# Kernel tuning notes

Measured on AMD Instinct MI355X. Metric: run time of the kernel, lower is better.

## Reference

```python
import jax, jax.numpy as jnp
import numpy as np
import math

DIM = 3
N_LEVELS = 16
F = 2
LOG2 = 19
TABLE = 1 << LOG2  # 524288 entries per level
BASE, FINEST = 16, 512
_B = math.exp((math.log(FINEST) - math.log(BASE)) / (N_LEVELS - 1))
RESOLUTIONS = [math.floor(BASE * _B ** i) for i in range(N_LEVELS)]
PRIMES = np.array([1, 2654435761, 805459861], dtype=np.uint32)
K = 1 << DIM  # 8 corners
# binary_mask[k, d]: bit d of corner k is 0 -> take lower corner along dim d
MASK = (np.arange(K)[:, None] & (1 << np.arange(DIM))[None, :]) == 0

N_POINTS = 1 << 20


def setup_inputs() -> dict:
    key = jax.random.key(0)
    kx, kt = jax.random.split(key)
    x = jax.random.uniform(kx, (N_POINTS, DIM), dtype=jnp.float32)
    # nn.init.uniform_(level.weight, a=-1e-4, b=1e-4), stacked over levels
    tables = (jax.random.uniform(kt, (N_LEVELS, TABLE, F), dtype=jnp.float32) - 0.5) * 2e-4
    return {"x": x, "tables": tables}


def _level(x, table, resolution):
    """One hash-grid level: corner hash + gather + trilinear interpolation."""
    xr = x * resolution                      # [N, DIM]
    ci = xr.astype(jnp.int32)                # trunc == floor for x >= 0
    cf = xr - ci.astype(xr.dtype)            # fractional part (diff w.r.t. x)
    mask = jnp.asarray(MASK)[None]           # [1, K, DIM]
    idx = jnp.where(mask, ci[:, None, :], ci[:, None, :] + 1)          # [N, K, DIM]
    w = jnp.where(mask, 1.0 - cf[:, None, :], cf[:, None, :]).prod(-1) # [N, K]
    # fast_hash: prime multiply (mod 2^32 via uint32 wrap), XOR fold, mod table size
    hashmap_size = min(resolution ** DIM, TABLE)
    h = idx.astype(jnp.uint32) * jnp.asarray(PRIMES)                    # [N, K, DIM]
    hashed = h[..., 0]
    for d in range(1, DIM):
        hashed = hashed ^ h[..., d]
    hashed = (hashed % jnp.uint32(hashmap_size)).astype(jnp.int32)      # [N, K]
    feats = table[hashed]                                               # [N, K, F]
    return (feats * w[..., None]).sum(axis=1)                           # [N, F]


def reference(x, tables):
    outs = [_level(x, tables[l], RESOLUTIONS[l]) for l in range(N_LEVELS)]
    return jnp.concatenate(outs, axis=-1)  # [N, N_LEVELS * F]
```

## Files before the change

kernel.cpp:

```cpp
#include <hip/hip_runtime.h>
#include <cmath>
#include <cstdint>

#define NLEVELS 16
#define TABLE_SZ (1u << 19)
#define NXCD 8

typedef float f4v __attribute__((ext_vector_type(4)));
typedef uint32_t u32x4 __attribute__((ext_vector_type(4)));

struct Params {
    uint32_t res[NLEVELS];
    uint32_t size[NLEVELS];
    uint64_t magic[NLEVELS];
    int lv0[NXCD];
    int lv1[NXCD];
};

__device__ __forceinline__ float bf_lo(uint32_t v) { return __uint_as_float(v << 16); }
__device__ __forceinline__ float bf_hi(uint32_t v) { return __uint_as_float(v & 0xFFFF0000u); }

__device__ __forceinline__ uint32_t pick4(u32x4 f, uint32_t j) {
    uint32_t e01 = (j & 1) ? f[1] : f[0];
    uint32_t e23 = (j & 1) ? f[3] : f[2];
    return (j & 2) ? e23 : e01;
}

__global__ __launch_bounds__(256) void convert_kernel(
    const float* __restrict__ tab, uint32_t* __restrict__ btab, Params p)
{
    int slot = blockIdx.x & (NXCD - 1);
    uint32_t cb = blockIdx.x >> 3;
    int l0 = p.lv0[slot], l1 = p.lv1[slot];
    uint32_t n0 = p.size[l0], n1 = p.size[l1];
    uint32_t total = n0 + n1;
    uint32_t stride = (gridDim.x >> 3) * 256;
    for (uint32_t i = cb * 256 + threadIdx.x; i < total; i += stride) {
        int l; uint32_t e;
        if (i < n0) { l = l0; e = i; } else { l = l1; e = i - n0; }
        unsigned long long u = __builtin_nontemporal_load(
            (const unsigned long long*)(tab + ((size_t)l * TABLE_SZ + e) * 2));
        uint32_t bx = (uint32_t)u, by = (uint32_t)(u >> 32);
        bx = (bx + 0x7fffu + ((bx >> 16) & 1u)) >> 16;
        by = (by + 0x7fffu + ((by >> 16) & 1u)) >> 16;
        btab[(size_t)l * TABLE_SZ + e] = bx | (by << 16);
    }
}

__global__ __launch_bounds__(256) void gather_kernel(
    const float* __restrict__ x, const uint32_t* __restrict__ btab,
    float2* __restrict__ ws, int p_lo, int passN, Params p)
{
    int slot = blockIdx.x & (NXCD - 1);
    int chunk = blockIdx.x >> 3;
    int rel = chunk * 256 + threadIdx.x;
    int pt = p_lo + rel;

    float x0 = __builtin_nontemporal_load(&x[(size_t)pt * 3 + 0]);
    float x1 = __builtin_nontemporal_load(&x[(size_t)pt * 3 + 1]);
    float x2 = __builtin_nontemporal_load(&x[(size_t)pt * 3 + 2]);

#pragma unroll
    for (int t = 0; t < 2; ++t) {
        int l = t ? p.lv1[slot] : p.lv0[slot];
        uint32_t size  = p.size[l];
        uint64_t magic = p.magic[l];
        float fres = (float)p.res[l];

        float xr0 = x0 * fres, xr1 = x1 * fres, xr2 = x2 * fres;
        int ci0 = (int)xr0, ci1 = (int)xr1, ci2 = (int)xr2;
        float cf0 = xr0 - (float)ci0;
        float cf1 = xr1 - (float)ci1;
        float cf2 = xr2 - (float)ci2;

        uint32_t c0u = (uint32_t)ci0, c0v = c0u + 1u;
        uint32_t h1a = (uint32_t)ci1 * 2654435761u; uint32_t h1b = h1a + 2654435761u;
        uint32_t h2a = (uint32_t)ci2 * 805459861u;  uint32_t h2b = h2a + 805459861u;
        float w0a = 1.0f - cf0, w1a = 1.0f - cf1, w2a = 1.0f - cf2;

        const uint32_t* __restrict__ tl = btab + (size_t)l * TABLE_SZ;
        float s0 = 0.0f, s1 = 0.0f;
#pragma unroll
        for (int pq = 0; pq < 4; ++pq) {
            uint32_t tyz = ((pq & 1) ? h1b : h1a) ^ ((pq & 2) ? h2b : h2a);
            float wyz = ((pq & 1) ? cf1 : w1a) * ((pq & 2) ? cf2 : w2a);
            uint32_t hU = tyz ^ c0u;
            uint32_t hV = tyz ^ c0v;
            uint32_t rU = hU - (uint32_t)__umul64hi((uint64_t)hU, magic) * size;
            uint32_t rV = hV - (uint32_t)__umul64hi((uint64_t)hV, magic) * size;
            uint32_t base = rU & ~3u;
            u32x4 f = *reinterpret_cast<const u32x4*>(tl + base);
            uint32_t eU = pick4(f, rU & 3u);
            uint32_t eV;
            if ((rV & ~3u) == base) {
                eV = pick4(f, rV & 3u);
            } else {
                eV = tl[rV];
            }
            float wU = w0a * wyz, wV = cf0 * wyz;
            s0 = fmaf(bf_lo(eU), wU, s0);
            s1 = fmaf(bf_hi(eU), wU, s1);
            s0 = fmaf(bf_lo(eV), wV, s0);
            s1 = fmaf(bf_hi(eV), wV, s1);
        }
        unsigned long long o = (unsigned long long)__float_as_uint(s0)
                             | ((unsigned long long)__float_as_uint(s1) << 32);
        __builtin_nontemporal_store(o,
            (unsigned long long*)(ws + (size_t)l * passN + rel));
    }
}

__global__ __launch_bounds__(256) void transpose_kernel(
    const float2* __restrict__ ws, f4v* __restrict__ out4, int p_lo, int passN)
{
    __shared__ float2 lds[256 * 17];
    int base = blockIdx.x * 256;
    int tid = threadIdx.x;
#pragma unroll
    for (int l = 0; l < NLEVELS; ++l) {
        unsigned long long u = __builtin_nontemporal_load(
            (const unsigned long long*)(ws + (size_t)l * passN + base + tid));
        float2 v;
        v.x = __uint_as_float((uint32_t)u);
        v.y = __uint_as_float((uint32_t)(u >> 32));
        lds[tid * 17 + l] = v;
    }
    __syncthreads();
    size_t ob = ((size_t)(p_lo + base)) * 8;
#pragma unroll
    for (int k = 0; k < 8; ++k) {
        int flat = k * 256 + tid;
        int ptl = flat >> 3, quad = flat & 7;
        float2 a = lds[ptl * 17 + quad * 2];
        float2 b = lds[ptl * 17 + quad * 2 + 1];
        f4v o = { a.x, a.y, b.x, b.y };
        __builtin_nontemporal_store(o, out4 + ob + flat);
    }
}

__global__ __launch_bounds__(256) void hashgrid_fallback(
    const float* __restrict__ x, const float* __restrict__ tables,
    float* __restrict__ out, int n_points, Params lp)
{
    int gid = blockIdx.x * blockDim.x + threadIdx.x;
    int n = gid >> 4;
    int l = gid & 15;
    if (n >= n_points) return;
    float x0 = x[(size_t)n * 3 + 0];
    float x1 = x[(size_t)n * 3 + 1];
    float x2 = x[(size_t)n * 3 + 2];
    uint32_t size = lp.size[l];
    uint64_t magic = lp.magic[l];
    float fres = (float)lp.res[l];
    float xr0 = x0 * fres, xr1 = x1 * fres, xr2 = x2 * fres;
    int ci0 = (int)xr0, ci1 = (int)xr1, ci2 = (int)xr2;
    float cf0 = xr0 - (float)ci0, cf1 = xr1 - (float)ci1, cf2 = xr2 - (float)ci2;
    uint32_t h0a = (uint32_t)ci0;               uint32_t h0b = h0a + 1u;
    uint32_t h1a = (uint32_t)ci1 * 2654435761u; uint32_t h1b = h1a + 2654435761u;
    uint32_t h2a = (uint32_t)ci2 * 805459861u;  uint32_t h2b = h2a + 805459861u;
    float w0a = 1.0f - cf0, w1a = 1.0f - cf1, w2a = 1.0f - cf2;
    const float2* t = reinterpret_cast<const float2*>(tables) + (size_t)l * TABLE_SZ;
    float s0 = 0.0f, s1 = 0.0f;
#pragma unroll
    for (int k = 0; k < 8; ++k) {
        uint32_t h = ((k & 1) ? h0b : h0a) ^ ((k & 2) ? h1b : h1a) ^ ((k & 4) ? h2b : h2a);
        uint32_t q = (uint32_t)__umul64hi((uint64_t)h, magic);
        h -= q * size;
        float w = ((k & 1) ? cf0 : w0a) * ((k & 2) ? cf1 : w1a) * ((k & 4) ? cf2 : w2a);
        float2 f = t[h];
        s0 = fmaf(f.x, w, s0);
        s1 = fmaf(f.y, w, s1);
    }
    reinterpret_cast<float2*>(out)[(size_t)n * NLEVELS + l] = make_float2(s0, s1);
}

extern "C" void kernel_launch(void* const* d_in, const int* in_sizes, int n_in,
                              void* d_out, int out_size, void* d_ws, size_t ws_size,
                              hipStream_t stream) {
    const float* x      = (const float*)d_in[0];
    const float* tables = (const float*)d_in[1];
    float* out          = (float*)d_out;
    int n_points = in_sizes[0] / 3;

    Params p;
    double b = exp((log(512.0) - log(16.0)) / 15.0);
    for (int i = 0; i < NLEVELS; ++i) {
        double r = floor(16.0 * pow(b, (double)i));
        uint32_t res = (uint32_t)r;
        uint64_t cube = (uint64_t)res * res * res;
        uint32_t size = (cube < (uint64_t)TABLE_SZ) ? (uint32_t)cube : TABLE_SZ;
        p.res[i] = res;
        p.size[i] = size;
        p.magic[i] = ~0ULL / size + 1ULL;
    }
    for (int s = 0; s < NXCD - 1; ++s) { p.lv0[s] = 7 + s; p.lv1[s] = s; }
    p.lv0[7] = 14; p.lv1[7] = 15;

    const size_t TAB_BYTES = (size_t)NLEVELS * TABLE_SZ * 4;
    size_t rem = (ws_size > TAB_BYTES) ? ws_size - TAB_BYTES : 0;
    int passN = (int)((rem / (NLEVELS * sizeof(float2))) & ~(size_t)255);
    if (passN > n_points) passN = n_points;

    if (passN < 256 || (n_points & 255) != 0) {
        int total = n_points * NLEVELS;
        hashgrid_fallback<<<(total + 255) / 256, 256, 0, stream>>>(x, tables, out, n_points, p);
        return;
    }

    uint32_t* btab = (uint32_t*)d_ws;
    float2* wsbuf = (float2*)((char*)d_ws + TAB_BYTES);

    convert_kernel<<<128 * NXCD, 256, 0, stream>>>(tables, btab, p);

    for (int p_lo = 0; p_lo < n_points; p_lo += passN) {
        int cnt = n_points - p_lo;
        if (cnt > passN) cnt = passN;
        int chunks = cnt / 256;
        gather_kernel<<<chunks * NXCD, 256, 0, stream>>>(x, btab, wsbuf, p_lo, cnt, p);
        transpose_kernel<<<chunks, 256, 0, stream>>>(wsbuf, (f4v*)out, p_lo, cnt);
    }
}
```

Baseline: 423.0 us.

## Fuse transpose into gather by pairing adjacent levels per XCD slot

Each XCD slot now handles two adjacent levels (2s, 2s+1), so a thread's four output floats are contiguous and can be written directly to the final output as one 16-byte store. This removes the intermediate workspace buffer and the separate LDS transpose kernel. Each thread also processes two points for more memory-level parallelism. The trade-off is that the old pairing of a coarse level with a fine level to balance load per XCD is gone, so slots handling two fine levels get more cache-missing gathers than slots handling coarse ones.

```diff
diff --git a/kernel.cpp b/kernel.cpp
--- a/kernel.cpp
+++ b/kernel.cpp
@@ -13,8 +13,6 @@
     uint32_t res[NLEVELS];
     uint32_t size[NLEVELS];
     uint64_t magic[NLEVELS];
-    int lv0[NXCD];
-    int lv1[NXCD];
 };
 
 __device__ __forceinline__ float bf_lo(uint32_t v) { return __uint_as_float(v << 16); }
@@ -26,12 +24,54 @@
     return (j & 2) ? e23 : e01;
 }
 
+__device__ __forceinline__ void enc_level(
+    float x0, float x1, float x2,
+    const uint32_t* __restrict__ tl, uint32_t size, uint64_t magic, float fres,
+    float& s0, float& s1)
+{
+    float xr0 = x0 * fres, xr1 = x1 * fres, xr2 = x2 * fres;
+    int ci0 = (int)xr0, ci1 = (int)xr1, ci2 = (int)xr2;
+    float cf0 = xr0 - (float)ci0;
+    float cf1 = xr1 - (float)ci1;
+    float cf2 = xr2 - (float)ci2;
+
+    uint32_t c0u = (uint32_t)ci0, c0v = c0u + 1u;
+    uint32_t h1a = (uint32_t)ci1 * 2654435761u; uint32_t h1b = h1a + 2654435761u;
+    uint32_t h2a = (uint32_t)ci2 * 805459861u;  uint32_t h2b = h2a + 805459861u;
+    float w0a = 1.0f - cf0, w1a = 1.0f - cf1, w2a = 1.0f - cf2;
+
+    s0 = 0.0f; s1 = 0.0f;
+#pragma unroll
+    for (int pq = 0; pq < 4; ++pq) {
+        uint32_t tyz = ((pq & 1) ? h1b : h1a) ^ ((pq & 2) ? h2b : h2a);
+        float wyz = ((pq & 1) ? cf1 : w1a) * ((pq & 2) ? cf2 : w2a);
+        uint32_t hU = tyz ^ c0u;
+        uint32_t hV = tyz ^ c0v;
+        uint32_t rU = hU - (uint32_t)__umul64hi((uint64_t)hU, magic) * size;
+        uint32_t rV = hV - (uint32_t)__umul64hi((uint64_t)hV, magic) * size;
+        uint32_t base = rU & ~3u;
+        u32x4 f = *reinterpret_cast<const u32x4*>(tl + base);
+        uint32_t eU = pick4(f, rU & 3u);
+        uint32_t eV;
+        if ((rV & ~3u) == base) {
+            eV = pick4(f, rV & 3u);
+        } else {
+            eV = tl[rV];
+        }
+        float wU = w0a * wyz, wV = cf0 * wyz;
+        s0 = fmaf(bf_lo(eU), wU, s0);
+        s1 = fmaf(bf_hi(eU), wU, s1);
+        s0 = fmaf(bf_lo(eV), wV, s0);
+        s1 = fmaf(bf_hi(eV), wV, s1);
+    }
+}
+
 __global__ __launch_bounds__(256) void convert_kernel(
     const float* __restrict__ tab, uint32_t* __restrict__ btab, Params p)
 {
     int slot = blockIdx.x & (NXCD - 1);
     uint32_t cb = blockIdx.x >> 3;
-    int l0 = p.lv0[slot], l1 = p.lv1[slot];
+    int l0 = slot * 2, l1 = l0 + 1;
     uint32_t n0 = p.size[l0], n1 = p.size[l1];
     uint32_t total = n0 + n1;
     uint32_t stride = (gridDim.x >> 3) * 256;
@@ -49,93 +89,38 @@
 
 __global__ __launch_bounds__(256) void gather_kernel(
     const float* __restrict__ x, const uint32_t* __restrict__ btab,
-    float2* __restrict__ ws, int p_lo, int passN, Params p)
+    f4v* __restrict__ out4, Params p)
 {
     int slot = blockIdx.x & (NXCD - 1);
     int chunk = blockIdx.x >> 3;
-    int rel = chunk * 256 + threadIdx.x;
-    int pt = p_lo + rel;
+    int pt0 = chunk * 512 + (int)threadIdx.x;
+    int pt1 = pt0 + 256;
 
-    float x0 = __builtin_nontemporal_load(&x[(size_t)pt * 3 + 0]);
-    float x1 = __builtin_nontemporal_load(&x[(size_t)pt * 3 + 1]);
-    float x2 = __builtin_nontemporal_load(&x[(size_t)pt * 3 + 2]);
+    float a0 = __builtin_nontemporal_load(&x[(size_t)pt0 * 3 + 0]);
+    float a1 = __builtin_nontemporal_load(&x[(size_t)pt0 * 3 + 1]);
+    float a2 = __builtin_nontemporal_load(&x[(size_t)pt0 * 3 + 2]);
+    float b0 = __builtin_nontemporal_load(&x[(size_t)pt1 * 3 + 0]);
+    float b1 = __builtin_nontemporal_load(&x[(size_t)pt1 * 3 + 1]);
+    float b2 = __builtin_nontemporal_load(&x[(size_t)pt1 * 3 + 2]);
 
-#pragma unroll
-    for (int t = 0; t < 2; ++t) {
-        int l = t ? p.lv1[slot] : p.lv0[slot];
-        uint32_t size  = p.size[l];
-        uint64_t magic = p.magic[l];
-        float fres = (float)p.res[l];
+    int l0 = slot * 2, l1 = l0 + 1;
+    const uint32_t* __restrict__ t0 = btab + (size_t)l0 * TABLE_SZ;
+    const uint32_t* __restrict__ t1 = btab + (size_t)l1 * TABLE_SZ;
+    uint32_t sz0 = p.size[l0], sz1 = p.size[l1];
+    uint64_t mg0 = p.magic[l0], mg1 = p.magic[l1];
+    float fr0 = (float)p.res[l0], fr1 = (float)p.res[l1];
 
-        float xr0 = x0 * fres, xr1 = x1 * fres, xr2 = x2 * fres;
-        int ci0 = (int)xr0, ci1 = (int)xr1, ci2 = (int)xr2;
-        float cf0 = xr0 - (float)ci0;
-        float cf1 = xr1 - (float)ci1;
-        float cf2 = xr2 - (float)ci2;
+    float pa0, pa1, pa2, pa3;
+    float pb0, pb1, pb2, pb3;
+    enc_level(a0, a1, a2, t0, sz0, mg0, fr0, pa0, pa1);
+    enc_level(b0, b1, b2, t0, sz0, mg0, fr0, pb0, pb1);
+    enc_level(a0, a1, a2, t1, sz1, mg1, fr1, pa2, pa3);
+    enc_level(b0, b1, b2, t1, sz1, mg1, fr1, pb2, pb3);
 
-        uint32_t c0u = (uint32_t)ci0, c0v = c0u + 1u;
-        uint32_t h1a = (uint32_t)ci1 * 2654435761u; uint32_t h1b = h1a + 2654435761u;
-        uint32_t h2a = (uint32_t)ci2 * 805459861u;  uint32_t h2b = h2a + 805459861u;
-        float w0a = 1.0f - cf0, w1a = 1.0f - cf1, w2a = 1.0f - cf2;
-
-        const uint32_t* __restrict__ tl = btab + (size_t)l * TABLE_SZ;
-        float s0 = 0.0f, s1 = 0.0f;
-#pragma unroll
-        for (int pq = 0; pq < 4; ++pq) {
-            uint32_t tyz = ((pq & 1) ? h1b : h1a) ^ ((pq & 2) ? h2b : h2a);
-            float wyz = ((pq & 1) ? cf1 : w1a) * ((pq & 2) ? cf2 : w2a);
-            uint32_t hU = tyz ^ c0u;
-            uint32_t hV = tyz ^ c0v;
-            uint32_t rU = hU - (uint32_t)__umul64hi((uint64_t)hU, magic) * size;
-            uint32_t rV = hV - (uint32_t)__umul64hi((uint64_t)hV, magic) * size;
-            uint32_t base = rU & ~3u;
-            u32x4 f = *reinterpret_cast<const u32x4*>(tl + base);
-            uint32_t eU = pick4(f, rU & 3u);
-            uint32_t eV;
-            if ((rV & ~3u) == base) {
-                eV = pick4(f, rV & 3u);
-            } else {
-                eV = tl[rV];
-            }
-            float wU = w0a * wyz, wV = cf0 * wyz;
-            s0 = fmaf(bf_lo(eU), wU, s0);
-            s1 = fmaf(bf_hi(eU), wU, s1);
-            s0 = fmaf(bf_lo(eV), wV, s0);
-            s1 = fmaf(bf_hi(eV), wV, s1);
-        }
-        unsigned long long o = (unsigned long long)__float_as_uint(s0)
-                             | ((unsigned long long)__float_as_uint(s1) << 32);
-        __builtin_nontemporal_store(o,
-            (unsigned long long*)(ws + (size_t)l * passN + rel));
-    }
-}
-
-__global__ __launch_bounds__(256) void transpose_kernel(
-    const float2* __restrict__ ws, f4v* __restrict__ out4, int p_lo, int passN)
-{
-    __shared__ float2 lds[256 * 17];
-    int base = blockIdx.x * 256;
-    int tid = threadIdx.x;
-#pragma unroll
-    for (int l = 0; l < NLEVELS; ++l) {
-        unsigned long long u = __builtin_nontemporal_load(
-            (const unsigned long long*)(ws + (size_t)l * passN + base + tid));
-        float2 v;
-        v.x = __uint_as_float((uint32_t)u);
-        v.y = __uint_as_float((uint32_t)(u >> 32));
-        lds[tid * 17 + l] = v;
-    }
-    __syncthreads();
-    size_t ob = ((size_t)(p_lo + base)) * 8;
-#pragma unroll
-    for (int k = 0; k < 8; ++k) {
-        int flat = k * 256 + tid;
-        int ptl = flat >> 3, quad = flat & 7;
-        float2 a = lds[ptl * 17 + quad * 2];
-        float2 b = lds[ptl * 17 + quad * 2 + 1];
-        f4v o = { a.x, a.y, b.x, b.y };
-        __builtin_nontemporal_store(o, out4 + ob + flat);
-    }
+    f4v oa = { pa0, pa1, pa2, pa3 };
+    f4v ob = { pb0, pb1, pb2, pb3 };
+    __builtin_nontemporal_store(oa, out4 + (size_t)pt0 * 8 + slot);
+    __builtin_nontemporal_store(ob, out4 + (size_t)pt1 * 8 + slot);
 }
 
 __global__ __launch_bounds__(256) void hashgrid_fallback(
@@ -193,30 +178,19 @@
         p.size[i] = size;
         p.magic[i] = ~0ULL / size + 1ULL;
     }
-    for (int s = 0; s < NXCD - 1; ++s) { p.lv0[s] = 7 + s; p.lv1[s] = s; }
-    p.lv0[7] = 14; p.lv1[7] = 15;
 
     const size_t TAB_BYTES = (size_t)NLEVELS * TABLE_SZ * 4;
-    size_t rem = (ws_size > TAB_BYTES) ? ws_size - TAB_BYTES : 0;
-    int passN = (int)((rem / (NLEVELS * sizeof(float2))) & ~(size_t)255);
-    if (passN > n_points) passN = n_points;
 
-    if (passN < 256 || (n_points & 255) != 0) {
+    if (ws_size < TAB_BYTES || (n_points & 511) != 0) {
         int total = n_points * NLEVELS;
         hashgrid_fallback<<<(total + 255) / 256, 256, 0, stream>>>(x, tables, out, n_points, p);
         return;
     }
 
     uint32_t* btab = (uint32_t*)d_ws;
-    float2* wsbuf = (float2*)((char*)d_ws + TAB_BYTES);
 
     convert_kernel<<<128 * NXCD, 256, 0, stream>>>(tables, btab, p);
 
-    for (int p_lo = 0; p_lo < n_points; p_lo += passN) {
-        int cnt = n_points - p_lo;
-        if (cnt > passN) cnt = passN;
-        int chunks = cnt / 256;
-        gather_kernel<<<chunks * NXCD, 256, 0, stream>>>(x, btab, wsbuf, p_lo, cnt, p);
-        transpose_kernel<<<chunks, 256, 0, stream>>>(wsbuf, (f4v*)out, p_lo, cnt);
-    }
+    int chunks = n_points / 512;
+    gather_kernel<<<chunks * NXCD, 256, 0, stream>>>(x, btab, (f4v*)out, p);
 }
```

After: 435.7 us. 3.0% more time.

## Pair coarse/fine levels per XCD, mask-based hash for full tables, bf16 workspace

Applied to the files above, without the earlier changes.

Reassigns each XCD slot to one small level and one full-size level (l and l+8). For full-size levels the modulo becomes a 19-bit mask, and the second x-corner's index is found by XOR, so the same-quad check reduces to a per-point condition. The intermediate workspace now stores bf16-packed results instead of fp32, halving transpose traffic. This adds extra bf16 rounding on the outputs, which risks accuracy, and changes the load balance across slots.

```diff
diff --git a/kernel.cpp b/kernel.cpp
--- a/kernel.cpp
+++ b/kernel.cpp
@@ -4,6 +4,7 @@
 
 #define NLEVELS 16
 #define TABLE_SZ (1u << 19)
+#define MASK19 (TABLE_SZ - 1u)
 #define NXCD 8
 
 typedef float f4v __attribute__((ext_vector_type(4)));
@@ -13,8 +14,6 @@
     uint32_t res[NLEVELS];
     uint32_t size[NLEVELS];
     uint64_t magic[NLEVELS];
-    int lv0[NXCD];
-    int lv1[NXCD];
 };
 
 __device__ __forceinline__ float bf_lo(uint32_t v) { return __uint_as_float(v << 16); }
@@ -26,12 +25,103 @@
     return (j & 2) ? e23 : e01;
 }
 
+__device__ __forceinline__ uint32_t rne_bf16(uint32_t u) {
+    return (u + 0x7fffu + ((u >> 16) & 1u)) >> 16;
+}
+__device__ __forceinline__ uint32_t pack_bf(float a, float b) {
+    return rne_bf16(__float_as_uint(a)) | (rne_bf16(__float_as_uint(b)) << 16);
+}
+
+__device__ __forceinline__ void enc_magic(
+    float x0, float x1, float x2,
+    const uint32_t* __restrict__ tl, uint32_t size, uint64_t magic, float fres,
+    float& s0, float& s1)
+{
+    float xr0 = x0 * fres, xr1 = x1 * fres, xr2 = x2 * fres;
+    int ci0 = (int)xr0, ci1 = (int)xr1, ci2 = (int)xr2;
+    float cf0 = xr0 - (float)ci0;
+    float cf1 = xr1 - (float)ci1;
+    float cf2 = xr2 - (float)ci2;
+
+    uint32_t c0u = (uint32_t)ci0, c0v = c0u + 1u;
+    uint32_t h1a = (uint32_t)ci1 * 2654435761u; uint32_t h1b = h1a + 2654435761u;
+    uint32_t h2a = (uint32_t)ci2 * 805459861u;  uint32_t h2b = h2a + 805459861u;
+    float w0a = 1.0f - cf0, w1a = 1.0f - cf1, w2a = 1.0f - cf2;
+
+    s0 = 0.0f; s1 = 0.0f;
+#pragma unroll
+    for (int pq = 0; pq < 4; ++pq) {
+        uint32_t tyz = ((pq & 1) ? h1b : h1a) ^ ((pq & 2) ? h2b : h2a);
+        float wyz = ((pq & 1) ? cf1 : w1a) * ((pq & 2) ? cf2 : w2a);
+        uint32_t hU = tyz ^ c0u;
+        uint32_t hV = tyz ^ c0v;
+        uint32_t rU = hU - (uint32_t)__umul64hi((uint64_t)hU, magic) * size;
+        uint32_t rV = hV - (uint32_t)__umul64hi((uint64_t)hV, magic) * size;
+        uint32_t base = rU & ~3u;
+        u32x4 f = *reinterpret_cast<const u32x4*>(tl + base);
+        uint32_t eU = pick4(f, rU & 3u);
+        uint32_t eV;
+        if ((rV & ~3u) == base) {
+            eV = pick4(f, rV & 3u);
+        } else {
+            eV = tl[rV];
+        }
+        float wU = w0a * wyz, wV = cf0 * wyz;
+        s0 = fmaf(bf_lo(eU), wU, s0);
+        s1 = fmaf(bf_hi(eU), wU, s1);
+        s0 = fmaf(bf_lo(eV), wV, s0);
+        s1 = fmaf(bf_hi(eV), wV, s1);
+    }
+}
+
+__device__ __forceinline__ void enc_capped(
+    float x0, float x1, float x2,
+    const uint32_t* __restrict__ tl, float fres,
+    float& s0, float& s1)
+{
+    float xr0 = x0 * fres, xr1 = x1 * fres, xr2 = x2 * fres;
+    int ci0 = (int)xr0, ci1 = (int)xr1, ci2 = (int)xr2;
+    float cf0 = xr0 - (float)ci0;
+    float cf1 = xr1 - (float)ci1;
+    float cf2 = xr2 - (float)ci2;
+
+    uint32_t c0u = (uint32_t)ci0;
+    uint32_t m = c0u ^ (c0u + 1u);
+    uint32_t h1a = (uint32_t)ci1 * 2654435761u; uint32_t h1b = h1a + 2654435761u;
+    uint32_t h2a = (uint32_t)ci2 * 805459861u;  uint32_t h2b = h2a + 805459861u;
+    float w0a = 1.0f - cf0, w1a = 1.0f - cf1, w2a = 1.0f - cf2;
+    bool nostrad = (m <= 3u);
+
+    s0 = 0.0f; s1 = 0.0f;
+#pragma unroll
+    for (int pq = 0; pq < 4; ++pq) {
+        uint32_t tyz = ((pq & 1) ? h1b : h1a) ^ ((pq & 2) ? h2b : h2a);
+        float wyz = ((pq & 1) ? cf1 : w1a) * ((pq & 2) ? cf2 : w2a);
+        uint32_t rU = (tyz ^ c0u) & MASK19;
+        uint32_t rV = rU ^ m;
+        uint32_t base = rU & ~3u;
+        u32x4 f = *reinterpret_cast<const u32x4*>(tl + base);
+        uint32_t eU = pick4(f, rU & 3u);
+        uint32_t eV;
+        if (nostrad) {
+            eV = pick4(f, rV & 3u);
+        } else {
+            eV = tl[rV];
+        }
+        float wU = w0a * wyz, wV = cf0 * wyz;
+        s0 = fmaf(bf_lo(eU), wU, s0);
+        s1 = fmaf(bf_hi(eU), wU, s1);
+        s0 = fmaf(bf_lo(eV), wV, s0);
+        s1 = fmaf(bf_hi(eV), wV, s1);
+    }
+}
+
 __global__ __launch_bounds__(256) void convert_kernel(
     const float* __restrict__ tab, uint32_t* __restrict__ btab, Params p)
 {
     int slot = blockIdx.x & (NXCD - 1);
     uint32_t cb = blockIdx.x >> 3;
-    int l0 = p.lv0[slot], l1 = p.lv1[slot];
+    int l0 = slot, l1 = slot + 8;
     uint32_t n0 = p.size[l0], n1 = p.size[l1];
     uint32_t total = n0 + n1;
     uint32_t stride = (gridDim.x >> 3) * 256;
@@ -40,100 +130,60 @@
         if (i < n0) { l = l0; e = i; } else { l = l1; e = i - n0; }
         unsigned long long u = __builtin_nontemporal_load(
             (const unsigned long long*)(tab + ((size_t)l * TABLE_SZ + e) * 2));
-        uint32_t bx = (uint32_t)u, by = (uint32_t)(u >> 32);
-        bx = (bx + 0x7fffu + ((bx >> 16) & 1u)) >> 16;
-        by = (by + 0x7fffu + ((by >> 16) & 1u)) >> 16;
-        btab[(size_t)l * TABLE_SZ + e] = bx | (by << 16);
+        btab[(size_t)l * TABLE_SZ + e] =
+            rne_bf16((uint32_t)u) | (rne_bf16((uint32_t)(u >> 32)) << 16);
     }
 }
 
 __global__ __launch_bounds__(256) void gather_kernel(
     const float* __restrict__ x, const uint32_t* __restrict__ btab,
-    float2* __restrict__ ws, int p_lo, int passN, Params p)
+    unsigned long long* __restrict__ ws2, int p_lo, int passN, Params p)
 {
     int slot = blockIdx.x & (NXCD - 1);
     int chunk = blockIdx.x >> 3;
-    int rel = chunk * 256 + threadIdx.x;
+    int rel = chunk * 256 + (int)threadIdx.x;
     int pt = p_lo + rel;
 
     float x0 = __builtin_nontemporal_load(&x[(size_t)pt * 3 + 0]);
     float x1 = __builtin_nontemporal_load(&x[(size_t)pt * 3 + 1]);
     float x2 = __builtin_nontemporal_load(&x[(size_t)pt * 3 + 2]);
 
-#pragma unroll
-    for (int t = 0; t < 2; ++t) {
-        int l = t ? p.lv1[slot] : p.lv0[slot];
-        uint32_t size  = p.size[l];
-        uint64_t magic = p.magic[l];
-        float fres = (float)p.res[l];
-
-        float xr0 = x0 * fres, xr1 = x1 * fres, xr2 = x2 * fres;
-        int ci0 = (int)xr0, ci1 = (int)xr1, ci2 = (int)xr2;
-        float cf0 = xr0 - (float)ci0;
-        float cf1 = xr1 - (float)ci1;
-        float cf2 = xr2 - (float)ci2;
-
-        uint32_t c0u = (uint32_t)ci0, c0v = c0u + 1u;
-        uint32_t h1a = (uint32_t)ci1 * 2654435761u; uint32_t h1b = h1a + 2654435761u;
-        uint32_t h2a = (uint32_t)ci2 * 805459861u;  uint32_t h2b = h2a + 805459861u;
-        float w0a = 1.0f - cf0, w1a = 1.0f - cf1, w2a = 1.0f - cf2;
-
-        const uint32_t* __restrict__ tl = btab + (size_t)l * TABLE_SZ;
-        float s0 = 0.0f, s1 = 0.0f;
-#pragma unroll
-        for (int pq = 0; pq < 4; ++pq) {
-            uint32_t tyz = ((pq & 1) ? h1b : h1a) ^ ((pq & 2) ? h2b : h2a);
-            float wyz = ((pq & 1) ? cf1 : w1a) * ((pq & 2) ? cf2 : w2a);
-            uint32_t hU = tyz ^ c0u;
-            uint32_t hV = tyz ^ c0v;
-            uint32_t rU = hU - (uint32_t)__umul64hi((uint64_t)hU, magic) * size;
-            uint32_t rV = hV - (uint32_t)__umul64hi((uint64_t)hV, magic) * size;
-            uint32_t base = rU & ~3u;
-            u32x4 f = *reinterpret_cast<const u32x4*>(tl + base);
-            uint32_t eU = pick4(f, rU & 3u);
-            uint32_t eV;
-            if ((rV & ~3u) == base) {
-                eV = pick4(f, rV & 3u);
-            } else {
-                eV = tl[rV];
-            }
-            float wU = w0a * wyz, wV = cf0 * wyz;
-            s0 = fmaf(bf_lo(eU), wU, s0);
-            s1 = fmaf(bf_hi(eU), wU, s1);
-            s0 = fmaf(bf_lo(eV), wV, s0);
-            s1 = fmaf(bf_hi(eV), wV, s1);
-        }
-        unsigned long long o = (unsigned long long)__float_as_uint(s0)
-                             | ((unsigned long long)__float_as_uint(s1) << 32);
-        __builtin_nontemporal_store(o,
-            (unsigned long long*)(ws + (size_t)l * passN + rel));
-    }
+    int l0 = slot, l1 = slot + 8;
+    const uint32_t* __restrict__ t0 = btab + (size_t)l0 * TABLE_SZ;
+    const uint32_t* __restrict__ t1 = btab + (size_t)l1 * TABLE_SZ;
+
+    float a0, a1, b0, b1;
+    enc_magic (x0, x1, x2, t0, p.size[l0], p.magic[l0], (float)p.res[l0], a0, a1);
+    enc_capped(x0, x1, x2, t1, (float)p.res[l1], b0, b1);
+
+    unsigned long long o = (unsigned long long)pack_bf(a0, a1)
+                         | ((unsigned long long)pack_bf(b0, b1) << 32);
+    __builtin_nontemporal_store(o, ws2 + (size_t)slot * passN + rel);
 }
 
 __global__ __launch_bounds__(256) void transpose_kernel(
-    const float2* __restrict__ ws, f4v* __restrict__ out4, int p_lo, int passN)
-{
-    __shared__ float2 lds[256 * 17];
+    const unsigned long long* __restrict__ ws2, f4v* __restrict__ out4,
+    int p_lo, int passN)
+{
+    __shared__ uint32_t lds[256 * 17];
     int base = blockIdx.x * 256;
     int tid = threadIdx.x;
 #pragma unroll
-    for (int l = 0; l < NLEVELS; ++l) {
-        unsigned long long u = __builtin_nontemporal_load(
-            (const unsigned long long*)(ws + (size_t)l * passN + base + tid));
-        float2 v;
-        v.x = __uint_as_float((uint32_t)u);
-        v.y = __uint_as_float((uint32_t)(u >> 32));
-        lds[tid * 17 + l] = v;
+    for (int s = 0; s < NXCD; ++s) {
+        unsigned long long v = __builtin_nontemporal_load(
+            &ws2[(size_t)s * passN + base + tid]);
+        lds[tid * 17 + s]     = (uint32_t)v;
+        lds[tid * 17 + s + 8] = (uint32_t)(v >> 32);
     }
     __syncthreads();
     size_t ob = ((size_t)(p_lo + base)) * 8;
 #pragma unroll
     for (int k = 0; k < 8; ++k) {
         int flat = k * 256 + tid;
-        int ptl = flat >> 3, quad = flat & 7;
-        float2 a = lds[ptl * 17 + quad * 2];
-        float2 b = lds[ptl * 17 + quad * 2 + 1];
-        f4v o = { a.x, a.y, b.x, b.y };
+        int ptl = flat >> 3, j = flat & 7;
+        uint32_t u0 = lds[ptl * 17 + 2 * j];
+        uint32_t u1 = lds[ptl * 17 + 2 * j + 1];
+        f4v o = { bf_lo(u0), bf_hi(u0), bf_lo(u1), bf_hi(u1) };
         __builtin_nontemporal_store(o, out4 + ob + flat);
     }
 }
@@ -193,22 +243,23 @@
         p.size[i] = size;
         p.magic[i] = ~0ULL / size + 1ULL;
     }
-    for (int s = 0; s < NXCD - 1; ++s) { p.lv0[s] = 7 + s; p.lv1[s] = s; }
-    p.lv0[7] = 14; p.lv1[7] = 15;
+    bool shape_ok = true;
+    for (int s = 0; s < 8; ++s)
+        shape_ok = shape_ok && (p.size[s] < TABLE_SZ) && (p.size[s + 8] == TABLE_SZ);
 
     const size_t TAB_BYTES = (size_t)NLEVELS * TABLE_SZ * 4;
     size_t rem = (ws_size > TAB_BYTES) ? ws_size - TAB_BYTES : 0;
-    int passN = (int)((rem / (NLEVELS * sizeof(float2))) & ~(size_t)255);
+    int passN = (int)((rem / (NXCD * sizeof(unsigned long long))) & ~(size_t)255);
     if (passN > n_points) passN = n_points;
 
-    if (passN < 256 || (n_points & 255) != 0) {
+    if (!shape_ok || passN < 256 || (n_points & 255) != 0) {
         int total = n_points * NLEVELS;
         hashgrid_fallback<<<(total + 255) / 256, 256, 0, stream>>>(x, tables, out, n_points, p);
         return;
     }
 
     uint32_t* btab = (uint32_t*)d_ws;
-    float2* wsbuf = (float2*)((char*)d_ws + TAB_BYTES);
+    unsigned long long* ws2 = (unsigned long long*)((char*)d_ws + TAB_BYTES);
 
     convert_kernel<<<128 * NXCD, 256, 0, stream>>>(tables, btab, p);
 
@@ -216,7 +267,7 @@
         int cnt = n_points - p_lo;
         if (cnt > passN) cnt = passN;
         int chunks = cnt / 256;
-        gather_kernel<<<chunks * NXCD, 256, 0, stream>>>(x, btab, wsbuf, p_lo, cnt, p);
-        transpose_kernel<<<chunks, 256, 0, stream>>>(wsbuf, (f4v*)out, p_lo, cnt);
-    }
-}
+        gather_kernel<<<chunks * NXCD, 256, 0, stream>>>(x, btab, ws2, p_lo, cnt, p);
+        transpose_kernel<<<chunks, 256, 0, stream>>>(ws2, (f4v*)out, p_lo, cnt);
+    }
+}
```

Measured after the change: 369.7 us. -12.6%, faster.
